# Kernel tuning notes

Hardware: AMD Instinct MI355X
Metric: run time of the kernel (lower is better)

Reference implementation:

```python
import jax, jax.numpy as jnp
import numpy as np

FEATURES, NEURONS, THETA, TAU, H = 128, 512, 256, 1.0, 0.1
B, T = 64, 2048

def setup_inputs() -> dict:
    key = jax.random.key(0)
    ks = jax.random.split(key, 8)
    IN = FEATURES + NEURONS
    s = lambda n: 1.0 / np.sqrt(n)
    return {
        "I": jax.random.normal(ks[0], (B, T, FEATURES), dtype=jnp.float32),
        "W_ih": jax.random.uniform(ks[1], (THETA, IN), jnp.float32, -s(THETA), s(THETA)),
        "W_hh": jax.random.uniform(ks[2], (THETA, THETA), jnp.float32, -s(THETA), s(THETA)),
        "b_ih": jax.random.uniform(ks[3], (THETA,), jnp.float32, -s(THETA), s(THETA)),
        "b_hh": jax.random.uniform(ks[4], (THETA,), jnp.float32, -s(THETA), s(THETA)),
        "W_out": jax.random.uniform(ks[5], (NEURONS, THETA), jnp.float32, -s(THETA), s(THETA)),
        "b_out": jax.random.uniform(ks[6], (NEURONS,), jnp.float32, -s(THETA), s(THETA)),
        "A": jax.random.normal(ks[7], (NEURONS,), dtype=jnp.float32),
    }

def reference(I, W_ih, W_hh, b_ih, b_hh, W_out, b_out, A):
    batch = I.shape[0]
    x0 = jnp.zeros((batch, NEURONS), I.dtype)
    s0 = jnp.zeros((batch, THETA), I.dtype)

    def step(carry, I_t):
        x, s = carry
        cat = jnp.concatenate([x, I_t], axis=-1)            # [B, neurons+features]
        s_new = jnp.tanh(cat @ W_ih.T + b_ih + s @ W_hh.T + b_hh)  # single-step tanh RNN
        f = jax.nn.relu(s_new @ W_out.T + b_out)            # [B, neurons]
        # implicit-Euler ODE update
        x_next = (x + H * (f * A)) / (1.0 + H * (1.0 / TAU + f))
        return (x_next, s_new), x_next

    _, xs = jax.lax.scan(step, (x0, s0), jnp.swapaxes(I, 0, 1))  # [T, B, neurons]
    return jnp.swapaxes(xs, 0, 1)  # [B, T, neurons]
```

## Files before the change

### kernel.cpp

```cpp
#include <hip/hip_runtime.h>
#include <hip/hip_bf16.h>

#define TT 2048
typedef unsigned int uint32;
typedef unsigned long long uint64;

#define WREG_N   (4 * 88 * 512)
#define EXA_N    (2 * 64 * 4 * 256)

__device__ __forceinline__ float lo16(uint32 u) { return __uint_as_float(u << 16); }
__device__ __forceinline__ float hi16(uint32 u) { return __uint_as_float(u & 0xffff0000u); }

__device__ __forceinline__ uint32 packbf(float lo, float hi)
{
    __hip_bfloat16 a = __float2bfloat16(lo), b = __float2bfloat16(hi);
    unsigned short ua = *reinterpret_cast<unsigned short*>(&a);
    unsigned short ub = *reinterpret_cast<unsigned short*>(&b);
    return (uint32)ua | ((uint32)ub << 16);
}

__device__ __forceinline__ float getA(const float* W_ih, const float* W_hh,
                                      int g, int j, int k)
{
    if (k < 128) return W_ih[j * 640 + 128 * g + k];
    if (k < 192) return W_hh[j * 256 + 64 * g + (k - 128)];
    return W_ih[j * 640 + 512 + 32 * g + (k - 192)];
}

__global__ void prep_kernel(const float* __restrict__ W_ih,
                            const float* __restrict__ W_hh,
                            const float* __restrict__ W_out,
                            uint32* __restrict__ WREG,
                            uint64* __restrict__ exA)
{
    int idx = blockIdx.x * blockDim.x + threadIdx.x;
    if (idx < WREG_N) {
        int tid = idx & 511;
        int q   = idx >> 9;
        int g   = q / 88;
        int i   = q % 88;
        float lo, hi;
        if (i < 56) {
            int j = tid & 255, h = tid >> 8;
            int k0 = 2 * (56 * h + i);
            lo = getA(W_ih, W_hh, g, j, k0);
            hi = getA(W_ih, W_hh, g, j, k0 + 1);
        } else {
            int n = tid & 127, h4 = tid >> 7;
            int ii = i - 56;
            int k0 = 64 * h4 + 2 * ii;
            int gn = 128 * g + n;
            lo = W_out[gn * 256 + k0];
            hi = W_out[gn * 256 + k0 + 1];
        }
        WREG[idx] = packbf(lo, hi);
    } else if (idx < WREG_N + EXA_N) {
        exA[idx - WREG_N] = 0ULL;
    }
}

__device__ __forceinline__ void bar_lds()
{
    asm volatile("s_waitcnt lgkmcnt(0)" ::: "memory");
    __builtin_amdgcn_s_barrier();
    asm volatile("" ::: "memory");
}

__global__ __launch_bounds__(512)
void scan_kernel(const float* __restrict__ I,
                 const float* __restrict__ b_ih, const float* __restrict__ b_hh,
                 const float* __restrict__ b_out, const float* __restrict__ A,
                 const uint32* __restrict__ WREG,
                 uint64* exA,
                 float* __restrict__ out)
{
    __shared__ float aloc[224];
    __shared__ float sful[256];
    __shared__ float part[512];

    const int tid = threadIdx.x;
    const int bid = blockIdx.x;
    const int b   = bid & 63;
    const int g   = bid >> 6;

    uint32 wA[56], wB[32];
    const uint32* wsrc = WREG + (g * 88) * 512 + tid;
    #pragma unroll
    for (int i = 0; i < 56; ++i) wA[i] = wsrc[i * 512];
    #pragma unroll
    for (int i = 0; i < 32; ++i) wB[i] = wsrc[(56 + i) * 512];

    const int j  = tid & 255;
    const int h  = tid >> 8;
    const int h4 = tid >> 7;

    const float bs   = (tid < 256) ? (b_ih[j] + b_hh[j]) : 0.f;
    const float bo_r = (tid < 128) ? b_out[128 * g + tid] : 0.f;
    const float Av_r = (tid < 128) ? A[128 * g + tid] : 0.f;

    if (tid < 224) aloc[tid] = 0.f;
    const size_t iBase   = (size_t)b * TT * 128 + 32 * g;
    const size_t outBase = (size_t)b * TT * 512 + 128 * g;
    if (tid < 32) aloc[192 + tid] = I[iBase + tid];
    __syncthreads();

    const float4* aloc4 = (const float4*)aloc;
    const float4* s4    = (const float4*)sful;

    for (int t = 0; t < TT; ++t) {
        float iv = 0.f;
        if (tid < 32) {
            int tl = (t + 1 < TT) ? (t + 1) : t;
            iv = I[iBase + (size_t)tl * 128 + tid];
        }

        float a0 = 0.f, a1 = 0.f;
        #pragma unroll
        for (int i = 0; i < 28; ++i) {
            float4 av = aloc4[28 * h + i];
            uint32 w0 = wA[2 * i], w1 = wA[2 * i + 1];
            a0 = fmaf(av.x, lo16(w0), a0);
            a1 = fmaf(av.y, hi16(w0), a1);
            a0 = fmaf(av.z, lo16(w1), a0);
            a1 = fmaf(av.w, hi16(w1), a1);
        }
        part[tid] = a0 + a1;
        bar_lds();

        const int par = t & 1;
        uint64* ex = exA + (size_t)(par * 64 + b) * (4 * 256);
        const uint32 tgt = (uint32)(t + 1);

        if (tid < 256) {
            float p = part[tid] + part[tid + 256];
            uint64 u = ((uint64)tgt << 32) | (uint64)__float_as_uint(p);
            __hip_atomic_store(ex + g * 256 + tid, u,
                               __ATOMIC_RELAXED, __HIP_MEMORY_SCOPE_AGENT);

            float v0 = 0.f, v1 = 0.f, v2 = 0.f;
            uint32 got = 0;
            const int g1 = (g + 1) & 3, g2 = (g + 2) & 3, g3 = (g + 3) & 3;
            do {
                if (!(got & 1u)) {
                    uint64 u1 = __hip_atomic_load(ex + g1 * 256 + tid,
                                                  __ATOMIC_RELAXED, __HIP_MEMORY_SCOPE_AGENT);
                    if ((uint32)(u1 >> 32) == tgt) { v0 = __uint_as_float((uint32)u1); got |= 1u; }
                }
                if (!(got & 2u)) {
                    uint64 u2 = __hip_atomic_load(ex + g2 * 256 + tid,
                                                  __ATOMIC_RELAXED, __HIP_MEMORY_SCOPE_AGENT);
                    if ((uint32)(u2 >> 32) == tgt) { v1 = __uint_as_float((uint32)u2); got |= 2u; }
                }
                if (!(got & 4u)) {
                    uint64 u3 = __hip_atomic_load(ex + g3 * 256 + tid,
                                                  __ATOMIC_RELAXED, __HIP_MEMORY_SCOPE_AGENT);
                    if ((uint32)(u3 >> 32) == tgt) { v2 = __uint_as_float((uint32)u3); got |= 4u; }
                }
            } while (got != 7u);

            float pre = p + bs + v0 + v1 + v2;
            float e  = __expf(2.f * pre);
            float sn = 1.f - 2.f / (e + 1.f);
            sful[tid] = sn;
            int d = tid - 64 * g;
            if (d >= 0 && d < 64) aloc[128 + d] = sn;
        }
        bar_lds();

        float c0 = 0.f, c1 = 0.f;
        #pragma unroll
        for (int i = 0; i < 16; ++i) {
            float4 sv = s4[16 * h4 + i];
            uint32 w0 = wB[2 * i], w1 = wB[2 * i + 1];
            c0 = fmaf(sv.x, lo16(w0), c0);
            c1 = fmaf(sv.y, hi16(w0), c1);
            c0 = fmaf(sv.z, lo16(w1), c0);
            c1 = fmaf(sv.w, hi16(w1), c1);
        }
        part[tid] = c0 + c1;
        bar_lds();

        if (tid < 128) {
            float f = part[tid] + part[tid + 128] + part[tid + 256] + part[tid + 384] + bo_r;
            f = fmaxf(f, 0.f);
            float xo = aloc[tid];
            float xn = (xo + 0.1f * f * Av_r) / (1.1f + 0.1f * f);
            aloc[tid] = xn;
            out[outBase + (size_t)t * 512 + tid] = xn;
        }
        if (tid < 32) aloc[192 + tid] = iv;
        bar_lds();
    }
}

extern "C" void kernel_launch(void* const* d_in, const int* in_sizes, int n_in,
                              void* d_out, int out_size, void* d_ws, size_t ws_size,
                              hipStream_t stream)
{
    const float* I     = (const float*)d_in[0];
    const float* W_ih  = (const float*)d_in[1];
    const float* W_hh  = (const float*)d_in[2];
    const float* b_ih  = (const float*)d_in[3];
    const float* b_hh  = (const float*)d_in[4];
    const float* W_out = (const float*)d_in[5];
    const float* b_out = (const float*)d_in[6];
    const float* A     = (const float*)d_in[7];

    uint32* WREG = (uint32*)d_ws;
    uint64* exA  = (uint64*)((uint32*)d_ws + WREG_N);

    const int total = WREG_N + EXA_N;
    prep_kernel<<<(total + 1023) / 1024, 1024, 0, stream>>>(W_ih, W_hh, W_out, WREG, exA);
    scan_kernel<<<256, 512, 0, stream>>>(I, b_ih, b_hh, b_out, A,
                                         WREG, exA, (float*)d_out);
}
```

Measured before the change: 4.294 ms.

## Replace LDS partial-sum reductions with lane shuffles and double-buffer state

Weights are re-laid out so the split-K partners of each output are adjacent lanes, letting partial sums be combined with __shfl_xor instead of an LDS array plus an extra barrier. The per-step state vector is double-buffered by time parity, which removes the other intermediate barrier. W_out reads are rotated per lane to spread LDS bank accesses. This cuts two of four block barriers per timestep. In exchange, half or three quarters of the lanes sit idle in the spin-wait and update phases, and those phases now span all wavefronts instead of a few.

```diff
diff --git a/kernel.cpp b/kernel.cpp
--- a/kernel.cpp
+++ b/kernel.cpp
@@ -41,17 +41,19 @@
         int i   = q % 88;
         float lo, hi;
         if (i < 56) {
-            int j = tid & 255, h = tid >> 8;
-            int k0 = 2 * (56 * h + i);
+            int j = tid >> 1, h = tid & 1;
+            int k0 = 112 * h + 2 * i;
             lo = getA(W_ih, W_hh, g, j, k0);
             hi = getA(W_ih, W_hh, g, j, k0 + 1);
         } else {
-            int n = tid & 127, h4 = tid >> 7;
-            int ii = i - 56;
-            int k0 = 64 * h4 + 2 * ii;
-            int gn = 128 * g + n;
-            lo = W_out[gn * 256 + k0];
-            hi = W_out[gn * 256 + k0 + 1];
+            int p  = i - 56;
+            int s  = p >> 1, qq = p & 1;
+            int kq = tid & 3;
+            int n  = 128 * g + (tid >> 2);
+            int blk = (s + 2 * kq) & 15;
+            int k0  = 64 * kq + 4 * blk + 2 * qq;
+            lo = W_out[n * 256 + k0];
+            hi = W_out[n * 256 + k0 + 1];
         }
         WREG[idx] = packbf(lo, hi);
     } else if (idx < WREG_N + EXA_N) {
@@ -74,9 +76,8 @@
                  uint64* exA,
                  float* __restrict__ out)
 {
-    __shared__ float aloc[224];
-    __shared__ float sful[256];
-    __shared__ float part[512];
+    __shared__ float4 aloc4[2][56];
+    __shared__ float  sful[256];
 
     const int tid = threadIdx.x;
     const int bid = blockIdx.x;
@@ -90,24 +91,30 @@
     #pragma unroll
     for (int i = 0; i < 32; ++i) wB[i] = wsrc[(56 + i) * 512];
 
-    const int j  = tid & 255;
-    const int h  = tid >> 8;
-    const int h4 = tid >> 7;
-
-    const float bs   = (tid < 256) ? (b_ih[j] + b_hh[j]) : 0.f;
-    const float bo_r = (tid < 128) ? b_out[128 * g + tid] : 0.f;
-    const float Av_r = (tid < 128) ? A[128 * g + tid] : 0.f;
-
-    if (tid < 224) aloc[tid] = 0.f;
+    const int h  = tid & 1;
+    const int jA = tid >> 1;
+    const int kq = tid & 3;
+    const int nB = tid >> 2;
+
+    const float bs   = ((tid & 1) == 0) ? (b_ih[jA] + b_hh[jA]) : 0.f;
+    const float bo_r = ((tid & 3) == 0) ? b_out[128 * g + nB] : 0.f;
+    const float Av_r = ((tid & 3) == 0) ? A[128 * g + nB] : 0.f;
+
     const size_t iBase   = (size_t)b * TT * 128 + 32 * g;
     const size_t outBase = (size_t)b * TT * 512 + 128 * g;
-    if (tid < 32) aloc[192 + tid] = I[iBase + tid];
+
+    {
+        float* a0 = (float*)&aloc4[0][0];
+        if (tid < 192) a0[tid] = 0.f;
+        else if (tid < 224) a0[tid] = I[iBase + (tid - 192)];
+    }
     __syncthreads();
 
-    const float4* aloc4 = (const float4*)aloc;
-    const float4* s4    = (const float4*)sful;
-
     for (int t = 0; t < TT; ++t) {
+        const int par = t & 1;
+        const float4* rd = aloc4[par];
+        float*        wr = (float*)aloc4[par ^ 1];
+
         float iv = 0.f;
         if (tid < 32) {
             int tl = (t + 1 < TT) ? (t + 1) : t;
@@ -117,24 +124,22 @@
         float a0 = 0.f, a1 = 0.f;
         #pragma unroll
         for (int i = 0; i < 28; ++i) {
-            float4 av = aloc4[28 * h + i];
+            float4 av = rd[28 * h + i];
             uint32 w0 = wA[2 * i], w1 = wA[2 * i + 1];
             a0 = fmaf(av.x, lo16(w0), a0);
             a1 = fmaf(av.y, hi16(w0), a1);
             a0 = fmaf(av.z, lo16(w1), a0);
             a1 = fmaf(av.w, hi16(w1), a1);
         }
-        part[tid] = a0 + a1;
-        bar_lds();
-
-        const int par = t & 1;
+        float accA = a0 + a1;
+        accA += __shfl_xor(accA, 1);
+
+        const uint32 tgt = (uint32)(t + 1);
         uint64* ex = exA + (size_t)(par * 64 + b) * (4 * 256);
-        const uint32 tgt = (uint32)(t + 1);
-
-        if (tid < 256) {
-            float p = part[tid] + part[tid + 256];
-            uint64 u = ((uint64)tgt << 32) | (uint64)__float_as_uint(p);
-            __hip_atomic_store(ex + g * 256 + tid, u,
+
+        if ((tid & 1) == 0) {
+            uint64 u = ((uint64)tgt << 32) | (uint64)__float_as_uint(accA);
+            __hip_atomic_store(ex + g * 256 + jA, u,
                                __ATOMIC_RELAXED, __HIP_MEMORY_SCOPE_AGENT);
 
             float v0 = 0.f, v1 = 0.f, v2 = 0.f;
@@ -142,53 +147,55 @@
             const int g1 = (g + 1) & 3, g2 = (g + 2) & 3, g3 = (g + 3) & 3;
             do {
                 if (!(got & 1u)) {
-                    uint64 u1 = __hip_atomic_load(ex + g1 * 256 + tid,
+                    uint64 u1 = __hip_atomic_load(ex + g1 * 256 + jA,
                                                   __ATOMIC_RELAXED, __HIP_MEMORY_SCOPE_AGENT);
                     if ((uint32)(u1 >> 32) == tgt) { v0 = __uint_as_float((uint32)u1); got |= 1u; }
                 }
                 if (!(got & 2u)) {
-                    uint64 u2 = __hip_atomic_load(ex + g2 * 256 + tid,
+                    uint64 u2 = __hip_atomic_load(ex + g2 * 256 + jA,
                                                   __ATOMIC_RELAXED, __HIP_MEMORY_SCOPE_AGENT);
                     if ((uint32)(u2 >> 32) == tgt) { v1 = __uint_as_float((uint32)u2); got |= 2u; }
                 }
                 if (!(got & 4u)) {
-                    uint64 u3 = __hip_atomic_load(ex + g3 * 256 + tid,
+                    uint64 u3 = __hip_atomic_load(ex + g3 * 256 + jA,
                                                   __ATOMIC_RELAXED, __HIP_MEMORY_SCOPE_AGENT);
                     if ((uint32)(u3 >> 32) == tgt) { v2 = __uint_as_float((uint32)u3); got |= 4u; }
                 }
             } while (got != 7u);
 
-            float pre = p + bs + v0 + v1 + v2;
+            float pre = accA + bs + v0 + v1 + v2;
             float e  = __expf(2.f * pre);
             float sn = 1.f - 2.f / (e + 1.f);
-            sful[tid] = sn;
-            int d = tid - 64 * g;
-            if (d >= 0 && d < 64) aloc[128 + d] = sn;
+            sful[jA] = sn;
+            int d = jA - 64 * g;
+            if (d >= 0 && d < 64) wr[128 + d] = sn;
         }
         bar_lds();
 
+        const float4* s4 = (const float4*)sful;
         float c0 = 0.f, c1 = 0.f;
         #pragma unroll
-        for (int i = 0; i < 16; ++i) {
-            float4 sv = s4[16 * h4 + i];
-            uint32 w0 = wB[2 * i], w1 = wB[2 * i + 1];
+        for (int s2 = 0; s2 < 16; ++s2) {
+            int blk = (s2 + 2 * kq) & 15;
+            float4 sv = s4[16 * kq + blk];
+            uint32 w0 = wB[2 * s2], w1 = wB[2 * s2 + 1];
             c0 = fmaf(sv.x, lo16(w0), c0);
             c1 = fmaf(sv.y, hi16(w0), c1);
             c0 = fmaf(sv.z, lo16(w1), c0);
             c1 = fmaf(sv.w, hi16(w1), c1);
         }
-        part[tid] = c0 + c1;
-        bar_lds();
-
-        if (tid < 128) {
-            float f = part[tid] + part[tid + 128] + part[tid + 256] + part[tid + 384] + bo_r;
-            f = fmaxf(f, 0.f);
-            float xo = aloc[tid];
-            float xn = (xo + 0.1f * f * Av_r) / (1.1f + 0.1f * f);
-            aloc[tid] = xn;
-            out[outBase + (size_t)t * 512 + tid] = xn;
-        }
-        if (tid < 32) aloc[192 + tid] = iv;
+        float f = c0 + c1;
+        f += __shfl_xor(f, 1);
+        f += __shfl_xor(f, 2);
+
+        if ((tid & 3) == 0) {
+            float ff = fmaxf(f + bo_r, 0.f);
+            float xo = ((const float*)rd)[nB];
+            float xn = (xo + 0.1f * ff * Av_r) / (1.1f + 0.1f * ff);
+            wr[nB] = xn;
+            out[outBase + (size_t)t * 512 + nB] = xn;
+        }
+        if (tid < 32) wr[192 + tid] = iv;
         bar_lds();
     }
 }
```

Result: slower. 4.420 ms (+2.9%).
